# Kernel optimization log

Measured on AMD Instinct MI355X. Metric: run time of the kernel, lower is better.

Reference implementation:

```python
import jax, jax.numpy as jnp
import numpy as np

NUM_CODES = 8192
CODE_DEPTH = 64
D_MODEL = 1024
NUM_LEVELS = 1


def setup_inputs() -> dict:
    key = jax.random.key(0)
    k1, k2, k3, k4 = jax.random.split(key, 4)
    x = jax.random.normal(k1, (8, 2048, D_MODEL), dtype=jnp.float32)
    # nn.Linear(d_model, code_depth): weight [code_depth, d_model], bias [code_depth]
    W_down = jax.random.normal(k2, (CODE_DEPTH, D_MODEL), dtype=jnp.float32) * 0.02
    b_down = jnp.zeros((CODE_DEPTH,), dtype=jnp.float32)
    # codebook = torch.randn(num_levels, num_codes, code_depth)
    codebook = jax.random.normal(k3, (NUM_LEVELS, NUM_CODES, CODE_DEPTH), dtype=jnp.float32)
    return {"x": x, "W_down": W_down, "b_down": b_down, "codebook": codebook}


def reference(x, W_down, b_down, codebook):
    # downsample: Linear(d_model -> code_depth), level 0
    soft = jnp.einsum("bsd,cd->bsc", x, W_down) + b_down  # [B,S,C]
    book = codebook[0]  # [K,C]
    # cdist(x, book).argmin == argmin of squared distances (sqrt is monotone)
    x2 = jnp.sum(soft * soft, axis=-1, keepdims=True)      # [B,S,1]
    c2 = jnp.sum(book * book, axis=-1)                     # [K]
    xc = jnp.einsum("bsc,kc->bsk", soft, book)             # [B,S,K]
    sq_dist = x2 - 2.0 * xc + c2                           # [B,S,K]
    code_indices = jnp.argmin(sq_dist, axis=-1)            # [B,S] int
    hard = book[code_indices]                              # [B,S,C]
    # training-mode losses (mse_loss = mean over all elements)
    commitment_loss = jnp.mean((jax.lax.stop_gradient(hard) - soft) ** 2)
    embedding_loss = jnp.mean((hard - jax.lax.stop_gradient(soft)) ** 2)
    # straight-through estimator
    hard_ste = soft + jax.lax.stop_gradient(hard - soft)
    return (soft, code_indices, hard_ste, commitment_loss, embedding_loss)
```

## Files before the change

### kernel.cpp

```cpp
#include <hip/hip_runtime.h>

#define M_TOT   16384
#define DM      1024
#define CD      64
#define NCODES  8192

#define SOFT_OFF  0
#define IDX_OFF   1048576
#define HARD_OFF  1064960
#define LOSS_OFF  2113536

__global__ __launch_bounds__(256) void compute_c2(const float* __restrict__ book,
                                                  float* __restrict__ c2) {
    const int k = blockIdx.x * 256 + threadIdx.x;
    const float4* p = (const float4*)(book + (size_t)k * CD);
    float s = 0.0f;
#pragma unroll
    for (int q = 0; q < CD / 4; ++q) {
        const float4 v = p[q];
        s = fmaf(v.x, v.x, s);
        s = fmaf(v.y, v.y, s);
        s = fmaf(v.z, v.z, s);
        s = fmaf(v.w, v.w, s);
    }
    c2[k] = s;
}

__global__ __launch_bounds__(256) void soft_gemm(const float* __restrict__ x,
                                                 const float* __restrict__ W,
                                                 const float* __restrict__ bias,
                                                 float* __restrict__ out_soft) {
    __shared__ float xt[32][68];
    __shared__ float wt[32][68];

    const int tid = threadIdx.x;
    const int r0  = blockIdx.x * 64;
    const int cg  = tid & 15;
    const int rg  = tid >> 4;

    float acc[4][4] = {};

    for (int k0 = 0; k0 < DM; k0 += 32) {
#pragma unroll
        for (int i = 0; i < 2; ++i) {
            const int f   = tid + i * 256;
            const int row = f >> 3;
            const int kq  = (f & 7) * 4;
            const float4 v = *(const float4*)(x + (size_t)(r0 + row) * DM + k0 + kq);
            xt[kq + 0][row] = v.x; xt[kq + 1][row] = v.y;
            xt[kq + 2][row] = v.z; xt[kq + 3][row] = v.w;
            const float4 w = *(const float4*)(W + (size_t)row * DM + k0 + kq);
            wt[kq + 0][row] = w.x; wt[kq + 1][row] = w.y;
            wt[kq + 2][row] = w.z; wt[kq + 3][row] = w.w;
        }
        __syncthreads();
#pragma unroll 8
        for (int kk = 0; kk < 32; ++kk) {
            const float4 xv = *(const float4*)&xt[kk][rg * 4];
            const float4 wv = *(const float4*)&wt[kk][cg * 4];
            const float xa[4] = {xv.x, xv.y, xv.z, xv.w};
            const float wa[4] = {wv.x, wv.y, wv.z, wv.w};
#pragma unroll
            for (int r = 0; r < 4; ++r)
#pragma unroll
                for (int q = 0; q < 4; ++q)
                    acc[r][q] = fmaf(xa[r], wa[q], acc[r][q]);
        }
        __syncthreads();
    }

    const float4 bb = *(const float4*)(bias + cg * 4);
#pragma unroll
    for (int r = 0; r < 4; ++r) {
        float4 o;
        o.x = acc[r][0] + bb.x; o.y = acc[r][1] + bb.y;
        o.z = acc[r][2] + bb.z; o.w = acc[r][3] + bb.w;
        *(float4*)(out_soft + (size_t)(r0 + rg * 4 + r) * CD + cg * 4) = o;
    }
}

__global__ __launch_bounds__(256) void dist_argmin(const float* __restrict__ soft,
                                                   const float* __restrict__ book,
                                                   const float* __restrict__ c2,
                                                   float* __restrict__ cand_d,
                                                   int* __restrict__ cand_i) {
    __shared__ float st[64][68];
    __shared__ float bt[64][132];
    __shared__ float c2s[128];
    __shared__ float redd[16][64];
    __shared__ int   redi[16][64];

    const int tid   = threadIdx.x;
    const int r0    = blockIdx.x * 64;
    const int kbase = blockIdx.y * (NCODES / 2);

#pragma unroll
    for (int i = 0; i < 4; ++i) {
        const int f   = tid + i * 256;
        const int row = f >> 4;
        const int dq  = (f & 15) * 4;
        const float4 v = *(const float4*)(soft + (size_t)(r0 + row) * CD + dq);
        st[dq + 0][row] = v.x; st[dq + 1][row] = v.y;
        st[dq + 2][row] = v.z; st[dq + 3][row] = v.w;
    }

    const int rg = tid & 15;
    const int kg = tid >> 4;

    float mind[4] = {3.4e38f, 3.4e38f, 3.4e38f, 3.4e38f};
    int   mini[4] = {0, 0, 0, 0};

    for (int kt = 0; kt < NCODES / 2; kt += 128) {
#pragma unroll
        for (int i = 0; i < 8; ++i) {
            const int f    = tid + i * 256;
            const int code = f >> 4;
            const int dq   = (f & 15) * 4;
            const float4 v = *(const float4*)(book + (size_t)(kbase + kt + code) * CD + dq);
            bt[dq + 0][code] = v.x; bt[dq + 1][code] = v.y;
            bt[dq + 2][code] = v.z; bt[dq + 3][code] = v.w;
        }
        if (tid < 128) c2s[tid] = c2[kbase + kt + tid];
        __syncthreads();

        float acc[4][8] = {};
#pragma unroll 4
        for (int d = 0; d < 64; ++d) {
            const float4 s  = *(const float4*)&st[d][rg * 4];
            const float4 b0 = *(const float4*)&bt[d][kg * 8];
            const float4 b1 = *(const float4*)&bt[d][kg * 8 + 4];
            const float sv[4] = {s.x, s.y, s.z, s.w};
            const float bv[8] = {b0.x, b0.y, b0.z, b0.w, b1.x, b1.y, b1.z, b1.w};
#pragma unroll
            for (int r = 0; r < 4; ++r)
#pragma unroll
                for (int j = 0; j < 8; ++j)
                    acc[r][j] = fmaf(sv[r], bv[j], acc[r][j]);
        }
        __syncthreads();

#pragma unroll
        for (int j = 0; j < 8; ++j) {
            const int   kidx = kbase + kt + kg * 8 + j;
            const float cc   = c2s[kg * 8 + j];
#pragma unroll
            for (int r = 0; r < 4; ++r) {
                const float dd = fmaf(-2.0f, acc[r][j], cc);
                if (dd < mind[r]) { mind[r] = dd; mini[r] = kidx; }
            }
        }
    }

#pragma unroll
    for (int r = 0; r < 4; ++r) {
        redd[kg][rg * 4 + r] = mind[r];
        redi[kg][rg * 4 + r] = mini[r];
    }
    __syncthreads();
    if (tid < 64) {
        float bd = redd[0][tid];
        int   bi = redi[0][tid];
#pragma unroll
        for (int g = 1; g < 16; ++g) {
            const float dd = redd[g][tid];
            if (dd < bd) { bd = dd; bi = redi[g][tid]; }
        }
        cand_d[blockIdx.y * M_TOT + r0 + tid] = bd;
        cand_i[blockIdx.y * M_TOT + r0 + tid] = bi;
    }
}

__global__ __launch_bounds__(256) void finalize(const float* __restrict__ book,
                                                const float* __restrict__ cand_d,
                                                const int* __restrict__ cand_i,
                                                float* __restrict__ out) {
    __shared__ float red[256];
    const int tid = threadIdx.x;
    const int row = blockIdx.x * 16 + (tid >> 4);
    const int dq  = (tid & 15) * 4;

    const float d0 = cand_d[row];
    const float d1 = cand_d[M_TOT + row];
    const int   i0 = cand_i[row];
    const int   i1 = cand_i[M_TOT + row];
    const int   k  = (d1 < d0) ? i1 : i0;

    if (dq == 0) out[IDX_OFF + row] = (float)k;

    const float4 h = *(const float4*)(book + (size_t)k * CD + dq);
    const float4 s = *(const float4*)(out + SOFT_OFF + (size_t)row * CD + dq);

    const float dx = h.x - s.x, dy = h.y - s.y, dz = h.z - s.z, dw = h.w - s.w;
    float4 ste;
    ste.x = s.x + dx; ste.y = s.y + dy; ste.z = s.z + dz; ste.w = s.w + dw;
    *(float4*)(out + HARD_OFF + (size_t)row * CD + dq) = ste;

    red[tid] = dx * dx + dy * dy + dz * dz + dw * dw;
    __syncthreads();
#pragma unroll
    for (int sh = 128; sh > 0; sh >>= 1) {
        if (tid < sh) red[tid] += red[tid + sh];
        __syncthreads();
    }
    if (tid == 0) {
        const float v = red[0] * (1.0f / (float)(M_TOT * CD));
        atomicAdd(out + LOSS_OFF, v);
        atomicAdd(out + LOSS_OFF + 1, v);
    }
}

extern "C" void kernel_launch(void* const* d_in, const int* in_sizes, int n_in,
                              void* d_out, int out_size, void* d_ws, size_t ws_size,
                              hipStream_t stream) {
    const float* x    = (const float*)d_in[0];
    const float* W    = (const float*)d_in[1];
    const float* bias = (const float*)d_in[2];
    const float* book = (const float*)d_in[3];
    float* out = (float*)d_out;

    float* ws     = (float*)d_ws;
    float* c2     = ws;
    float* cand_d = ws + NCODES;
    int*   cand_i = (int*)(ws + NCODES + 2 * M_TOT);

    compute_c2<<<NCODES / 256, 256, 0, stream>>>(book, c2);
    soft_gemm<<<M_TOT / 64, 256, 0, stream>>>(x, W, bias, out + SOFT_OFF);
    dist_argmin<<<dim3(M_TOT / 64, 2), 256, 0, stream>>>(out + SOFT_OFF, book, c2,
                                                         cand_d, cand_i);
    hipMemsetAsync(out + LOSS_OFF, 0, 2 * sizeof(float), stream);
    finalize<<<M_TOT / 16, 256, 0, stream>>>(book, cand_d, cand_i, out);
}
```

Baseline: 458.9 us.

## Split-K soft GEMM and per-thread-row distance argmin across 16 code chunks

Splits the 1024-deep downsample GEMM into four K-chunks that write partial sums, with a separate reduce kernel adding them and the bias, so more blocks run in parallel. Replaces the shared-memory tiled distance kernel with one thread per row that keeps the row in registers and streams codebook rows from global memory. The codebook is split into 16 chunks instead of 2, and finalize reduces 16 candidates per row. This adds partial-buffer traffic and an extra launch. The new distance loop relies on wavefront-uniform codebook loads being cached, and it gives up the register tile reuse of the old kernel.

```diff
diff --git a/kernel.cpp b/kernel.cpp
--- a/kernel.cpp
+++ b/kernel.cpp
@@ -4,6 +4,8 @@
 #define DM      1024
 #define CD      64
 #define NCODES  8192
+#define NCHUNK  16
+#define CPC     (NCODES / NCHUNK)
 
 #define SOFT_OFF  0
 #define IDX_OFF   1048576
@@ -26,21 +28,23 @@
     c2[k] = s;
 }
 
-__global__ __launch_bounds__(256) void soft_gemm(const float* __restrict__ x,
-                                                 const float* __restrict__ W,
-                                                 const float* __restrict__ bias,
-                                                 float* __restrict__ out_soft) {
+__global__ __launch_bounds__(256) void soft_gemm_k(const float* __restrict__ x,
+                                                   const float* __restrict__ W,
+                                                   const float* __restrict__ bias,
+                                                   float* __restrict__ dst,
+                                                   int kchunk) {
     __shared__ float xt[32][68];
     __shared__ float wt[32][68];
 
     const int tid = threadIdx.x;
     const int r0  = blockIdx.x * 64;
+    const int k0base = blockIdx.y * kchunk;
     const int cg  = tid & 15;
     const int rg  = tid >> 4;
 
     float acc[4][4] = {};
 
-    for (int k0 = 0; k0 < DM; k0 += 32) {
+    for (int k0 = k0base; k0 < k0base + kchunk; k0 += 32) {
 #pragma unroll
         for (int i = 0; i < 2; ++i) {
             const int f   = tid + i * 256;
@@ -69,123 +73,121 @@
         __syncthreads();
     }
 
-    const float4 bb = *(const float4*)(bias + cg * 4);
+    float4 bb = make_float4(0.f, 0.f, 0.f, 0.f);
+    if (bias) bb = *(const float4*)(bias + cg * 4);
+    float* base = dst + (size_t)blockIdx.y * M_TOT * CD;
 #pragma unroll
     for (int r = 0; r < 4; ++r) {
         float4 o;
         o.x = acc[r][0] + bb.x; o.y = acc[r][1] + bb.y;
         o.z = acc[r][2] + bb.z; o.w = acc[r][3] + bb.w;
-        *(float4*)(out_soft + (size_t)(r0 + rg * 4 + r) * CD + cg * 4) = o;
-    }
-}
-
-__global__ __launch_bounds__(256) void dist_argmin(const float* __restrict__ soft,
-                                                   const float* __restrict__ book,
-                                                   const float* __restrict__ c2,
-                                                   float* __restrict__ cand_d,
-                                                   int* __restrict__ cand_i) {
-    __shared__ float st[64][68];
-    __shared__ float bt[64][132];
-    __shared__ float c2s[128];
-    __shared__ float redd[16][64];
-    __shared__ int   redi[16][64];
-
-    const int tid   = threadIdx.x;
-    const int r0    = blockIdx.x * 64;
-    const int kbase = blockIdx.y * (NCODES / 2);
-
-#pragma unroll
-    for (int i = 0; i < 4; ++i) {
-        const int f   = tid + i * 256;
-        const int row = f >> 4;
-        const int dq  = (f & 15) * 4;
-        const float4 v = *(const float4*)(soft + (size_t)(r0 + row) * CD + dq);
-        st[dq + 0][row] = v.x; st[dq + 1][row] = v.y;
-        st[dq + 2][row] = v.z; st[dq + 3][row] = v.w;
-    }
-
-    const int rg = tid & 15;
-    const int kg = tid >> 4;
-
-    float mind[4] = {3.4e38f, 3.4e38f, 3.4e38f, 3.4e38f};
-    int   mini[4] = {0, 0, 0, 0};
-
-    for (int kt = 0; kt < NCODES / 2; kt += 128) {
-#pragma unroll
-        for (int i = 0; i < 8; ++i) {
-            const int f    = tid + i * 256;
-            const int code = f >> 4;
-            const int dq   = (f & 15) * 4;
-            const float4 v = *(const float4*)(book + (size_t)(kbase + kt + code) * CD + dq);
-            bt[dq + 0][code] = v.x; bt[dq + 1][code] = v.y;
-            bt[dq + 2][code] = v.z; bt[dq + 3][code] = v.w;
-        }
-        if (tid < 128) c2s[tid] = c2[kbase + kt + tid];
-        __syncthreads();
-
-        float acc[4][8] = {};
-#pragma unroll 4
-        for (int d = 0; d < 64; ++d) {
-            const float4 s  = *(const float4*)&st[d][rg * 4];
-            const float4 b0 = *(const float4*)&bt[d][kg * 8];
-            const float4 b1 = *(const float4*)&bt[d][kg * 8 + 4];
-            const float sv[4] = {s.x, s.y, s.z, s.w};
-            const float bv[8] = {b0.x, b0.y, b0.z, b0.w, b1.x, b1.y, b1.z, b1.w};
-#pragma unroll
-            for (int r = 0; r < 4; ++r)
-#pragma unroll
-                for (int j = 0; j < 8; ++j)
-                    acc[r][j] = fmaf(sv[r], bv[j], acc[r][j]);
-        }
-        __syncthreads();
-
-#pragma unroll
-        for (int j = 0; j < 8; ++j) {
-            const int   kidx = kbase + kt + kg * 8 + j;
-            const float cc   = c2s[kg * 8 + j];
-#pragma unroll
-            for (int r = 0; r < 4; ++r) {
-                const float dd = fmaf(-2.0f, acc[r][j], cc);
-                if (dd < mind[r]) { mind[r] = dd; mini[r] = kidx; }
-            }
-        }
-    }
-
-#pragma unroll
-    for (int r = 0; r < 4; ++r) {
-        redd[kg][rg * 4 + r] = mind[r];
-        redi[kg][rg * 4 + r] = mini[r];
-    }
-    __syncthreads();
-    if (tid < 64) {
-        float bd = redd[0][tid];
-        int   bi = redi[0][tid];
-#pragma unroll
-        for (int g = 1; g < 16; ++g) {
-            const float dd = redd[g][tid];
-            if (dd < bd) { bd = dd; bi = redi[g][tid]; }
-        }
-        cand_d[blockIdx.y * M_TOT + r0 + tid] = bd;
-        cand_i[blockIdx.y * M_TOT + r0 + tid] = bi;
-    }
+        *(float4*)(base + (size_t)(r0 + rg * 4 + r) * CD + cg * 4) = o;
+    }
+}
+
+__global__ __launch_bounds__(256) void soft_reduce(const float* __restrict__ partial,
+                                                   const float* __restrict__ bias,
+                                                   float* __restrict__ out_soft,
+                                                   int nsplit) {
+    const int i = blockIdx.x * 256 + threadIdx.x;
+    const float4* p = (const float4*)partial;
+    float4 s = p[i];
+    for (int j = 1; j < nsplit; ++j) {
+        const float4 v = p[(size_t)j * (M_TOT * CD / 4) + i];
+        s.x += v.x; s.y += v.y; s.z += v.z; s.w += v.w;
+    }
+    const float4 bb = ((const float4*)bias)[i & 15];
+    s.x += bb.x; s.y += bb.y; s.z += bb.z; s.w += bb.w;
+    ((float4*)out_soft)[i] = s;
+}
+
+__global__ __launch_bounds__(256) void dist_argmin2(const float* __restrict__ soft,
+                                                    const float* __restrict__ book,
+                                                    const float* __restrict__ c2,
+                                                    float* __restrict__ cand_d,
+                                                    int* __restrict__ cand_i) {
+    const int row   = blockIdx.x * 256 + threadIdx.x;
+    const int kbase = blockIdx.y * CPC;
+
+    float4 s4[16];
+    const float4* sp = (const float4*)(soft + (size_t)row * CD);
+#pragma unroll
+    for (int q = 0; q < 16; ++q) s4[q] = sp[q];
+
+    float mind = 3.4e38f;
+    int   mini = kbase;
+    const float4* bp = (const float4*)(book + (size_t)kbase * CD);
+
+    for (int kk = 0; kk < CPC; kk += 4) {
+        const float4* b0 = bp + (size_t)(kk + 0) * 16;
+        const float4* b1 = bp + (size_t)(kk + 1) * 16;
+        const float4* b2 = bp + (size_t)(kk + 2) * 16;
+        const float4* b3 = bp + (size_t)(kk + 3) * 16;
+        float a0 = 0.f, a1 = 0.f, a2 = 0.f, a3 = 0.f;
+#pragma unroll
+        for (int q = 0; q < 16; ++q) {
+            const float4 sv = s4[q];
+            const float4 v0 = b0[q];
+            a0 = fmaf(sv.x, v0.x, a0); a0 = fmaf(sv.y, v0.y, a0);
+            a0 = fmaf(sv.z, v0.z, a0); a0 = fmaf(sv.w, v0.w, a0);
+            const float4 v1 = b1[q];
+            a1 = fmaf(sv.x, v1.x, a1); a1 = fmaf(sv.y, v1.y, a1);
+            a1 = fmaf(sv.z, v1.z, a1); a1 = fmaf(sv.w, v1.w, a1);
+            const float4 v2 = b2[q];
+            a2 = fmaf(sv.x, v2.x, a2); a2 = fmaf(sv.y, v2.y, a2);
+            a2 = fmaf(sv.z, v2.z, a2); a2 = fmaf(sv.w, v2.w, a2);
+            const float4 v3 = b3[q];
+            a3 = fmaf(sv.x, v3.x, a3); a3 = fmaf(sv.y, v3.y, a3);
+            a3 = fmaf(sv.z, v3.z, a3); a3 = fmaf(sv.w, v3.w, a3);
+        }
+        const int k = kbase + kk;
+        const float d0 = fmaf(-2.f, a0, c2[k + 0]);
+        const float d1 = fmaf(-2.f, a1, c2[k + 1]);
+        const float d2 = fmaf(-2.f, a2, c2[k + 2]);
+        const float d3 = fmaf(-2.f, a3, c2[k + 3]);
+        if (d0 < mind) { mind = d0; mini = k + 0; }
+        if (d1 < mind) { mind = d1; mini = k + 1; }
+        if (d2 < mind) { mind = d2; mini = k + 2; }
+        if (d3 < mind) { mind = d3; mini = k + 3; }
+    }
+
+    cand_d[blockIdx.y * M_TOT + row] = mind;
+    cand_i[blockIdx.y * M_TOT + row] = mini;
 }
 
 __global__ __launch_bounds__(256) void finalize(const float* __restrict__ book,
                                                 const float* __restrict__ cand_d,
                                                 const int* __restrict__ cand_i,
                                                 float* __restrict__ out) {
+    __shared__ float rd[256];
+    __shared__ int   ri[256];
+    __shared__ int   ksels[16];
     __shared__ float red[256];
-    const int tid = threadIdx.x;
-    const int row = blockIdx.x * 16 + (tid >> 4);
-    const int dq  = (tid & 15) * 4;
-
-    const float d0 = cand_d[row];
-    const float d1 = cand_d[M_TOT + row];
-    const int   i0 = cand_i[row];
-    const int   i1 = cand_i[M_TOT + row];
-    const int   k  = (d1 < d0) ? i1 : i0;
-
-    if (dq == 0) out[IDX_OFF + row] = (float)k;
+
+    const int tid  = threadIdx.x;
+    const int rloc = tid >> 4;
+    const int g    = tid & 15;
+    const int row  = blockIdx.x * 16 + rloc;
+
+    rd[tid] = cand_d[(size_t)g * M_TOT + row];
+    ri[tid] = cand_i[(size_t)g * M_TOT + row];
+    __syncthreads();
+
+    if (g == 0) {
+        float bd = rd[rloc * 16];
+        int   bi = ri[rloc * 16];
+#pragma unroll
+        for (int j = 1; j < 16; ++j) {
+            const float dd = rd[rloc * 16 + j];
+            if (dd < bd) { bd = dd; bi = ri[rloc * 16 + j]; }
+        }
+        ksels[rloc] = bi;
+        out[IDX_OFF + row] = (float)bi;
+    }
+    __syncthreads();
+
+    const int k  = ksels[rloc];
+    const int dq = g * 4;
 
     const float4 h = *(const float4*)(book + (size_t)k * CD + dq);
     const float4 s = *(const float4*)(out + SOFT_OFF + (size_t)row * CD + dq);
@@ -221,12 +223,25 @@
     float* ws     = (float*)d_ws;
     float* c2     = ws;
     float* cand_d = ws + NCODES;
-    int*   cand_i = (int*)(ws + NCODES + 2 * M_TOT);
+    int*   cand_i = (int*)(cand_d + NCHUNK * M_TOT);
+    float* partial = (float*)(cand_i + NCHUNK * M_TOT);
+
+    const size_t base_floats = NCODES + (size_t)2 * NCHUNK * M_TOT;
+    int splitk = 4;
+    if (ws_size < (base_floats + (size_t)splitk * M_TOT * CD) * sizeof(float))
+        splitk = 1;
 
     compute_c2<<<NCODES / 256, 256, 0, stream>>>(book, c2);
-    soft_gemm<<<M_TOT / 64, 256, 0, stream>>>(x, W, bias, out + SOFT_OFF);
-    dist_argmin<<<dim3(M_TOT / 64, 2), 256, 0, stream>>>(out + SOFT_OFF, book, c2,
-                                                         cand_d, cand_i);
+
+    if (splitk == 4) {
+        soft_gemm_k<<<dim3(M_TOT / 64, 4), 256, 0, stream>>>(x, W, nullptr, partial, DM / 4);
+        soft_reduce<<<M_TOT * CD / 4 / 256, 256, 0, stream>>>(partial, bias, out + SOFT_OFF, 4);
+    } else {
+        soft_gemm_k<<<dim3(M_TOT / 64, 1), 256, 0, stream>>>(x, W, bias, out + SOFT_OFF, DM);
+    }
+
+    dist_argmin2<<<dim3(M_TOT / 256, NCHUNK), 256, 0, stream>>>(out + SOFT_OFF, book, c2,
+                                                                cand_d, cand_i);
     hipMemsetAsync(out + LOSS_OFF, 0, 2 * sizeof(float), stream);
     finalize<<<M_TOT / 16, 256, 0, stream>>>(book, cand_d, cand_i, out);
 }
```

Result: slower. 531.1 us (+15.7%).
